# Kernel tuning notes

Measured on AMD Instinct MI355X. Metric: run time of the kernel, lower is better.

Reference implementation:

```python
import jax, jax.numpy as jnp
import numpy as np

N_NODES = 100000

def gcn_conv(h, row, col, w, W, b, n):
    # linear transform then symmetric-normalized weighted aggregation (PyG GCNConv)
    h = h @ W                                   # [N, F_out]
    deg = jax.ops.segment_sum(w, row, num_segments=n)          # weighted in-degree [N]
    dinv = jnp.where(deg > 0, jax.lax.rsqrt(deg), 0.0)
    norm = dinv[row] * w * dinv[col]            # [E]
    msg = norm[:, None] * h[col]                # gather+scale, [E, F_out]
    return jax.ops.segment_sum(msg, row, num_segments=n) + b

def setup_inputs() -> dict:
    key = jax.random.key(0)
    ks = jax.random.split(key, 6)
    N, E, D, H = N_NODES, 1600000, 128, 128
    x = jax.random.normal(ks[0], (N, D), dtype=jnp.float32)
    edge_index = jax.random.randint(ks[1], (2, E), 0, N, dtype=jnp.int64)
    edge_weight = jax.random.uniform(ks[2], (E,), dtype=jnp.float32)
    W1 = jax.random.normal(ks[3], (D, H), dtype=jnp.float32) / np.sqrt(D)
    b1 = jnp.zeros((H,), dtype=jnp.float32)
    W2 = jax.random.normal(ks[4], (H, H), dtype=jnp.float32) / np.sqrt(H)
    b2 = jnp.zeros((H,), dtype=jnp.float32)
    return {"x": x, "edge_index": edge_index, "edge_weight": edge_weight,
            "W1": W1, "b1": b1, "W2": W2, "b2": b2}

def reference(x, edge_index, edge_weight, W1, b1, W2, b2):
    n = x.shape[0]
    # add self-loops with weight 1 (PyG gcn_norm default)
    loops = jnp.arange(n, dtype=edge_index.dtype)
    row = jnp.concatenate([edge_index[0], loops])
    col = jnp.concatenate([edge_index[1], loops])
    w = jnp.concatenate([edge_weight, jnp.ones((n,), dtype=edge_weight.dtype)])
    h = gcn_conv(x, row, col, w, W1, b1, n)
    h = jax.nn.relu(h)  # dropout is identity in eval mode
    h = gcn_conv(h, row, col, w, W2, b2, n)
    return h
```

## Files before the change

kernel.cpp:

```cpp
#include <hip/hip_runtime.h>


constexpr int N_NODES = 100000;
constexpr int FD = 128;
constexpr int NPAD = 100352;
constexpr int CAP = 48;
constexpr int PSH = 7;
constexpr int PROWS = 128;
constexpr int NP = (N_NODES + PROWS - 1) / PROWS;
constexpr int RCAP = 2560;
constexpr int PSTRIDE = 16;
constexpr int EPB = 4096;
constexpr int EPT = 16;

typedef __attribute__((ext_vector_type(8))) short bf16x8;
typedef __attribute__((ext_vector_type(4))) float f32x4;
#define MFMA16(a, b, c) __builtin_amdgcn_mfma_f32_16x16x32_bf16(a, b, c, 0, 0, 0)

static __device__ __forceinline__ unsigned f2bf(float x) {
  unsigned u = __float_as_uint(x);
  return (u + 0x7FFFu + ((u >> 16) & 1u)) >> 16;
}
static __device__ __forceinline__ float bflo(unsigned u) {
  return __uint_as_float(u << 16);
}
static __device__ __forceinline__ float bfhi(unsigned u) {
  return __uint_as_float(u & 0xFFFF0000u);
}

__global__ __launch_bounds__(256) void k_part(const int* __restrict__ row,
                                              const int* __restrict__ col,
                                              const float* __restrict__ w,
                                              int* __restrict__ pcnt,
                                              int2* __restrict__ rec, int E) {
  __shared__ int lcnt[NP];
  const int t = threadIdx.x;
  const int e0 = blockIdx.x * EPB;
  for (int p = t; p < NP; p += 256) lcnt[p] = 0;
  __syncthreads();

  int packed[EPT];
  int cols[EPT];
  int ws[EPT];
#pragma unroll
  for (int i = 0; i < EPT; i++) {
    int e = e0 + i * 256 + t;
    packed[i] = -1;
    if (e < E) {
      int r = row[e];
      cols[i] = col[e];
      ws[i] = __float_as_int(w[e]);
      int part = r >> PSH, rl = r & (PROWS - 1);
      int off = atomicAdd(&lcnt[part], 1);
      packed[i] = part | (rl << 10) | (off << 17);
    }
  }
  __syncthreads();

  for (int p = t; p < NP; p += 256) {
    int c = lcnt[p];
    int base = 0;
    if (c) base = atomicAdd(&pcnt[p * PSTRIDE], c);
    lcnt[p] = base;
  }
  __syncthreads();

#pragma unroll
  for (int i = 0; i < EPT; i++) {
    int pk = packed[i];
    if (pk >= 0) {
      int part = pk & 0x3FF;
      int rl = (pk >> 10) & 0x7F;
      int pos = lcnt[part] + (pk >> 17);
      if (pos < RCAP)
        rec[(size_t)part * RCAP + pos] = make_int2(cols[i] | (rl << 20), ws[i]);
    }
  }
}

__global__ __launch_bounds__(256) void k_bin(const int* __restrict__ pcnt,
                                             const int2* __restrict__ rec,
                                             int2* __restrict__ bucket,
                                             int* __restrict__ cnt,
                                             float* __restrict__ dinv) {
  __shared__ int lcnt[PROWS];
  __shared__ float lsum[PROWS];
  const int part = blockIdx.x, t = threadIdx.x;
  if (t < PROWS) { lcnt[t] = 0; lsum[t] = 0.f; }
  __syncthreads();
  const int n = min(pcnt[part * PSTRIDE], RCAP);
  const int row0 = part << PSH;
  const int2* rp = rec + (size_t)part * RCAP;
  for (int j = t; j < n; j += 256) {
    int2 R = rp[j];
    int rl = R.x >> 20;
    int c = R.x & 0xFFFFF;
    int p = atomicAdd(&lcnt[rl], 1);
    if (p < CAP) bucket[(size_t)(row0 + rl) * CAP + p] = make_int2(c, R.y);
    atomicAdd(&lsum[rl], __int_as_float(R.y));
  }
  __syncthreads();
  int i = row0 + t;
  if (t < PROWS && i < N_NODES) {
    cnt[i] = min(lcnt[t], CAP);
    dinv[i] = rsqrtf(lsum[t] + 1.0f);
  }
}

__global__ __launch_bounds__(128) void k_prep(const float* __restrict__ W1,
                                              const float* __restrict__ W2,
                                              ushort* __restrict__ W1hT,
                                              ushort* __restrict__ W1lT,
                                              ushort* __restrict__ W2hT,
                                              ushort* __restrict__ W2lT) {
  int b = blockIdx.x;
  int n0 = b & (FD - 1);
  int k = threadIdx.x;
  const float* W = (b < FD) ? W1 : W2;
  ushort* Wh = (b < FD) ? W1hT : W2hT;
  ushort* Wl = (b < FD) ? W1lT : W2lT;
  float v = W[k * FD + n0];
  unsigned h = f2bf(v);
  float r = v - bflo(h);
  Wh[n0 * FD + k] = (ushort)h;
  Wl[n0 * FD + k] = (ushort)f2bf(r);
}

__global__ __launch_bounds__(512) void k_gemm(const float* __restrict__ X,
                                              const ushort* __restrict__ WhT,
                                              const ushort* __restrict__ WlT,
                                              const float* __restrict__ dinv,
                                              ushort* __restrict__ Yb,
                                              int relu_in) {
  __shared__ ushort sl[32768];
  ushort* lwh = sl;
  ushort* lwl = sl + 16384;
  const int t = threadIdx.x;
  const int wid = t >> 6;
  const int lane = t & 63;
  const int g = lane >> 4;
  const int lr = lane & 15;

  const size_t row_base = (size_t)blockIdx.x * 128 + wid * 16 + lr;
  const size_t rowc = row_base < N_NODES ? row_base : 0;
  const float* xr = X + rowc * FD;
  float xv[4][8];
#pragma unroll
  for (int ks = 0; ks < 4; ks++) {
    *(float4*)&xv[ks][0] = *(const float4*)(xr + ks * 32 + g * 8);
    *(float4*)&xv[ks][4] = *(const float4*)(xr + ks * 32 + g * 8 + 4);
  }

  {
    const uint4* gh = (const uint4*)WhT;
    const uint4* gl = (const uint4*)WlT;
#pragma unroll
    for (int i = 0; i < 4; i++) {
      int idx = i * 512 + t;
      int byte = idx * 16;
      int n = byte >> 8;
      int swz = byte ^ ((n & 7) << 4);
      *(uint4*)((char*)lwh + swz) = gh[idx];
      *(uint4*)((char*)lwl + swz) = gl[idx];
    }
  }
  __syncthreads();

  f32x4 acc[8];
#pragma unroll
  for (int nf = 0; nf < 8; nf++) acc[nf] = (f32x4)(0.f);

#pragma unroll
  for (int ks = 0; ks < 4; ks++) {
    bf16x8 a_h, a_l;
#pragma unroll
    for (int j = 0; j < 8; j++) {
      float v = xv[ks][j];
      if (relu_in) v = fmaxf(v, 0.f);
      unsigned hb_ = f2bf(v);
      float r = v - bflo(hb_);
      a_h[j] = (short)hb_;
      a_l[j] = (short)f2bf(r);
    }
#pragma unroll
    for (int nf = 0; nf < 8; nf++) {
      int n = nf * 16 + lr;
      int byte = n * 256 + ks * 64 + g * 16;
      int swz = byte ^ ((n & 7) << 4);
      bf16x8 bh = *(const bf16x8*)((const char*)lwh + swz);
      bf16x8 bl = *(const bf16x8*)((const char*)lwl + swz);
      acc[nf] = MFMA16(a_h, bh, acc[nf]);
      acc[nf] = MFMA16(a_l, bh, acc[nf]);
      acc[nf] = MFMA16(a_h, bl, acc[nf]);
    }
  }

  float4 dv = *(const float4*)&dinv[blockIdx.x * 128 + wid * 16 + g * 4];

  __syncthreads();
#pragma unroll
  for (int nf = 0; nf < 8; nf++) {
#pragma unroll
    for (int r = 0; r < 4; r++) {
      int rl = wid * 16 + g * 4 + r;
      int byte = rl * 256 + (nf * 16 + lr) * 2;
      int swz = byte ^ ((rl & 7) << 4);
      *(ushort*)((char*)sl + swz) = (ushort)f2bf(acc[nf][r] * (&dv.x)[r]);
    }
  }
  __syncthreads();
#pragma unroll
  for (int i = 0; i < 4; i++) {
    int idx = i * 512 + t;
    int byte = idx * 16;
    int rl = byte >> 8;
    int swz = byte ^ ((rl & 7) << 4);
    uint4 v = *(const uint4*)((const char*)sl + swz);
    size_t rg = (size_t)blockIdx.x * 128 + rl;
    if (rg < N_NODES) *(uint4*)(Yb + rg * FD + ((byte & 255) >> 1)) = v;
  }
}

static __device__ __forceinline__ void acc8(float* a, float s, uint4 g) {
  a[0] += s * bflo(g.x);
  a[1] += s * bfhi(g.x);
  a[2] += s * bflo(g.y);
  a[3] += s * bfhi(g.y);
  a[4] += s * bflo(g.z);
  a[5] += s * bfhi(g.z);
  a[6] += s * bflo(g.w);
  a[7] += s * bfhi(g.w);
}

__global__ __launch_bounds__(256, 4) void k_gather(
    const ushort* __restrict__ hb, const int* __restrict__ cnt,
    const int2* __restrict__ bucket, const float* __restrict__ dinv,
    const float* __restrict__ b, float* __restrict__ out) {
  int t = blockIdx.x * 256 + threadIdx.x;
  int i = t >> 4, q = t & 15;
  if (i >= N_NODES) return;
  float di = dinv[i];
  const uint4* H = (const uint4*)hb;
  uint4 hv = H[(size_t)i * 16 + q];
  float a[8];
  a[0] = bflo(hv.x); a[1] = bfhi(hv.x);
  a[2] = bflo(hv.y); a[3] = bfhi(hv.y);
  a[4] = bflo(hv.z); a[5] = bfhi(hv.z);
  a[6] = bflo(hv.w); a[7] = bfhi(hv.w);
  const int c = min(cnt[i], CAP);
  const int2* bk = bucket + (size_t)i * CAP;
  const int nb = (c + 7) >> 3;

  int2 cur[8];
  if (nb > 0) {
#pragma unroll
    for (int j = 0; j < 4; j++)
      *(int4*)&cur[j * 2] = *(const int4*)&bk[j * 2];
  }
  for (int bt = 0; bt < nb; bt++) {
    int2 nxt[8];
    if (bt + 1 < nb) {
#pragma unroll
      for (int j = 0; j < 4; j++)
        *(int4*)&nxt[j * 2] = *(const int4*)&bk[(bt + 1) * 8 + j * 2];
    }
    const int base = bt * 8;
    int idx[8];
    float wv[8];
#pragma unroll
    for (int j = 0; j < 8; j++) {
      bool v = (base + j) < c;
      idx[j] = v ? cur[j].x : i;
      wv[j] = v ? __int_as_float(cur[j].y) : 0.f;
    }
    uint4 g[8];
#pragma unroll
    for (int j = 0; j < 8; j++) g[j] = H[(size_t)idx[j] * 16 + q];
#pragma unroll
    for (int j = 0; j < 8; j++) acc8(a, wv[j], g[j]);
#pragma unroll
    for (int j = 0; j < 8; j++) cur[j] = nxt[j];
  }
  float4 b0 = ((const float4*)b)[q * 2];
  float4 b1 = ((const float4*)b)[q * 2 + 1];
  float* o = out + (size_t)i * FD + q * 8;
  float4 o0, o1;
  o0.x = di * a[0] + b0.x; o0.y = di * a[1] + b0.y;
  o0.z = di * a[2] + b0.z; o0.w = di * a[3] + b0.w;
  o1.x = di * a[4] + b1.x; o1.y = di * a[5] + b1.y;
  o1.z = di * a[6] + b1.z; o1.w = di * a[7] + b1.w;
  ((float4*)o)[0] = o0;
  ((float4*)o)[1] = o1;
}

extern "C" void kernel_launch(void* const* d_in, const int* in_sizes, int n_in,
                              void* d_out, int out_size, void* d_ws, size_t ws_size,
                              hipStream_t stream) {
  const float* x  = (const float*)d_in[0];
  const int*   ei = (const int*)d_in[1];
  const float* ew = (const float*)d_in[2];
  const float* W1 = (const float*)d_in[3];
  const float* b1 = (const float*)d_in[4];
  const float* W2 = (const float*)d_in[5];
  const float* b2 = (const float*)d_in[6];
  float* out = (float*)d_out;

  const int E = in_sizes[2];
  const int* row = ei;
  const int* col = ei + E;

  int*    pcnt   = (int*)d_ws;
  float*  dinv   = (float*)(pcnt + 16384);
  int*    cnt    = (int*)(dinv + NPAD);
  int2*   bucket = (int2*)(cnt + NPAD);
  int2*   rec    = bucket + (size_t)NPAD * CAP;
  ushort* hb     = (ushort*)(rec + (size_t)NP * RCAP);
  ushort* w1ht   = hb + (size_t)NPAD * FD;
  ushort* w1lt   = w1ht + FD * FD;
  ushort* w2ht   = w1lt + FD * FD;
  ushort* w2lt   = w2ht + FD * FD;

  hipMemsetAsync(pcnt, 0, 16384 * sizeof(int), stream);
  k_prep<<<2 * FD, FD, 0, stream>>>(W1, W2, w1ht, w1lt, w2ht, w2lt);
  const int part_grid = (E + EPB - 1) / EPB;
  k_part<<<part_grid, 256, 0, stream>>>(row, col, ew, pcnt, rec, E);
  k_bin<<<NP, 256, 0, stream>>>(pcnt, rec, bucket, cnt, dinv);

  const int gemm_grid = (N_NODES + 127) / 128;
  const int ga_grid   = (N_NODES * 16 + 255) / 256;

  k_gemm<<<gemm_grid, 512, 0, stream>>>(x, w1ht, w1lt, dinv, hb, 0);
  k_gather<<<ga_grid, 256, 0, stream>>>(hb, cnt, bucket, dinv, b1, out);
  k_gemm<<<gemm_grid, 512, 0, stream>>>(out, w2ht, w2lt, dinv, hb, 1);
  k_gather<<<ga_grid, 256, 0, stream>>>(hb, cnt, bucket, dinv, b2, out);
}
```

Before: 335.1 us.

## Process two row tiles per GEMM block and store outputs directly with permuted columns

The GEMM kernel now handles 256 rows per block in two 128-row tiles, so each block's weight staging into LDS is reused twice. The B-fragment column mapping is permuted (n = lr*8 + nf) so that each lane holds 8 consecutive output columns. This lets the epilogue pack them into a uint4 and write straight to global memory, removing the LDS staging pass and its two barriers. The separate memset of the partition counters is folded into the weight-prep kernel, dropping one launch. The trade-off is half as many GEMM blocks, which lowers parallelism across CUs.

```diff
diff --git a/kernel.cpp b/kernel.cpp
--- a/kernel.cpp
+++ b/kernel.cpp
@@ -112,10 +112,13 @@
                                               ushort* __restrict__ W1hT,
                                               ushort* __restrict__ W1lT,
                                               ushort* __restrict__ W2hT,
-                                              ushort* __restrict__ W2lT) {
+                                              ushort* __restrict__ W2lT,
+                                              int* __restrict__ pcnt) {
   int b = blockIdx.x;
+  int k = threadIdx.x;
+  int zid = b * 128 + k;
+  if (zid < 16384) pcnt[zid] = 0;
   int n0 = b & (FD - 1);
-  int k = threadIdx.x;
   const float* W = (b < FD) ? W1 : W2;
   ushort* Wh = (b < FD) ? W1hT : W2hT;
   ushort* Wl = (b < FD) ? W1lT : W2lT;
@@ -141,16 +144,6 @@
   const int g = lane >> 4;
   const int lr = lane & 15;
 
-  const size_t row_base = (size_t)blockIdx.x * 128 + wid * 16 + lr;
-  const size_t rowc = row_base < N_NODES ? row_base : 0;
-  const float* xr = X + rowc * FD;
-  float xv[4][8];
-#pragma unroll
-  for (int ks = 0; ks < 4; ks++) {
-    *(float4*)&xv[ks][0] = *(const float4*)(xr + ks * 32 + g * 8);
-    *(float4*)&xv[ks][4] = *(const float4*)(xr + ks * 32 + g * 8 + 4);
-  }
-
   {
     const uint4* gh = (const uint4*)WhT;
     const uint4* gl = (const uint4*)WlT;
@@ -159,65 +152,69 @@
       int idx = i * 512 + t;
       int byte = idx * 16;
       int n = byte >> 8;
-      int swz = byte ^ ((n & 7) << 4);
+      int swz = byte ^ (((n >> 3) & 7) << 4);
       *(uint4*)((char*)lwh + swz) = gh[idx];
       *(uint4*)((char*)lwl + swz) = gl[idx];
     }
   }
   __syncthreads();
 
-  f32x4 acc[8];
-#pragma unroll
-  for (int nf = 0; nf < 8; nf++) acc[nf] = (f32x4)(0.f);
-
-#pragma unroll
-  for (int ks = 0; ks < 4; ks++) {
-    bf16x8 a_h, a_l;
-#pragma unroll
-    for (int j = 0; j < 8; j++) {
-      float v = xv[ks][j];
-      if (relu_in) v = fmaxf(v, 0.f);
-      unsigned hb_ = f2bf(v);
-      float r = v - bflo(hb_);
-      a_h[j] = (short)hb_;
-      a_l[j] = (short)f2bf(r);
-    }
-#pragma unroll
-    for (int nf = 0; nf < 8; nf++) {
-      int n = nf * 16 + lr;
-      int byte = n * 256 + ks * 64 + g * 16;
-      int swz = byte ^ ((n & 7) << 4);
-      bf16x8 bh = *(const bf16x8*)((const char*)lwh + swz);
-      bf16x8 bl = *(const bf16x8*)((const char*)lwl + swz);
-      acc[nf] = MFMA16(a_h, bh, acc[nf]);
-      acc[nf] = MFMA16(a_l, bh, acc[nf]);
-      acc[nf] = MFMA16(a_h, bl, acc[nf]);
-    }
-  }
-
-  float4 dv = *(const float4*)&dinv[blockIdx.x * 128 + wid * 16 + g * 4];
-
-  __syncthreads();
-#pragma unroll
-  for (int nf = 0; nf < 8; nf++) {
+#pragma unroll
+  for (int tile = 0; tile < 2; tile++) {
+    const size_t rb = (size_t)blockIdx.x * 256 + tile * 128;
+    const size_t row_base = rb + wid * 16 + lr;
+    const size_t rowc = row_base < N_NODES ? row_base : 0;
+    const float* xr = X + rowc * FD;
+    float xv[4][8];
+#pragma unroll
+    for (int ks = 0; ks < 4; ks++) {
+      *(float4*)&xv[ks][0] = *(const float4*)(xr + ks * 32 + g * 8);
+      *(float4*)&xv[ks][4] = *(const float4*)(xr + ks * 32 + g * 8 + 4);
+    }
+
+    f32x4 acc[8];
+#pragma unroll
+    for (int nf = 0; nf < 8; nf++) acc[nf] = (f32x4)(0.f);
+
+#pragma unroll
+    for (int ks = 0; ks < 4; ks++) {
+      bf16x8 a_h, a_l;
+#pragma unroll
+      for (int j = 0; j < 8; j++) {
+        float v = xv[ks][j];
+        if (relu_in) v = fmaxf(v, 0.f);
+        unsigned hb_ = f2bf(v);
+        float r = v - bflo(hb_);
+        a_h[j] = (short)hb_;
+        a_l[j] = (short)f2bf(r);
+      }
+#pragma unroll
+      for (int nf = 0; nf < 8; nf++) {
+        int n = lr * 8 + nf;
+        int byte = n * 256 + ks * 64 + g * 16;
+        int swz = byte ^ (((n >> 3) & 7) << 4);
+        bf16x8 bh = *(const bf16x8*)((const char*)lwh + swz);
+        bf16x8 bl = *(const bf16x8*)((const char*)lwl + swz);
+        acc[nf] = MFMA16(a_h, bh, acc[nf]);
+        acc[nf] = MFMA16(a_l, bh, acc[nf]);
+        acc[nf] = MFMA16(a_h, bl, acc[nf]);
+      }
+    }
+
+    const size_t rw = rb + wid * 16;
 #pragma unroll
     for (int r = 0; r < 4; r++) {
-      int rl = wid * 16 + g * 4 + r;
-      int byte = rl * 256 + (nf * 16 + lr) * 2;
-      int swz = byte ^ ((rl & 7) << 4);
-      *(ushort*)((char*)sl + swz) = (ushort)f2bf(acc[nf][r] * (&dv.x)[r]);
-    }
-  }
-  __syncthreads();
-#pragma unroll
-  for (int i = 0; i < 4; i++) {
-    int idx = i * 512 + t;
-    int byte = idx * 16;
-    int rl = byte >> 8;
-    int swz = byte ^ ((rl & 7) << 4);
-    uint4 v = *(const uint4*)((const char*)sl + swz);
-    size_t rg = (size_t)blockIdx.x * 128 + rl;
-    if (rg < N_NODES) *(uint4*)(Yb + rg * FD + ((byte & 255) >> 1)) = v;
+      size_t rg = rw + g * 4 + r;
+      if (rg < N_NODES) {
+        float dv = dinv[rg];
+        uint4 o;
+        o.x = f2bf(acc[0][r] * dv) | (f2bf(acc[1][r] * dv) << 16);
+        o.y = f2bf(acc[2][r] * dv) | (f2bf(acc[3][r] * dv) << 16);
+        o.z = f2bf(acc[4][r] * dv) | (f2bf(acc[5][r] * dv) << 16);
+        o.w = f2bf(acc[6][r] * dv) | (f2bf(acc[7][r] * dv) << 16);
+        *(uint4*)(Yb + rg * FD + lr * 8) = o;
+      }
+    }
   }
 }
 
@@ -320,13 +317,12 @@
   ushort* w2ht   = w1lt + FD * FD;
   ushort* w2lt   = w2ht + FD * FD;
 
-  hipMemsetAsync(pcnt, 0, 16384 * sizeof(int), stream);
-  k_prep<<<2 * FD, FD, 0, stream>>>(W1, W2, w1ht, w1lt, w2ht, w2lt);
+  k_prep<<<2 * FD, FD, 0, stream>>>(W1, W2, w1ht, w1lt, w2ht, w2lt, pcnt);
   const int part_grid = (E + EPB - 1) / EPB;
   k_part<<<part_grid, 256, 0, stream>>>(row, col, ew, pcnt, rec, E);
   k_bin<<<NP, 256, 0, stream>>>(pcnt, rec, bucket, cnt, dinv);
 
-  const int gemm_grid = (N_NODES + 127) / 128;
+  const int gemm_grid = (N_NODES + 255) / 256;
   const int ga_grid   = (N_NODES * 16 + 255) / 256;
 
   k_gemm<<<gemm_grid, 512, 0, stream>>>(x, w1ht, w1lt, dinv, hb, 0);
```

Result: faster. 322.8 us (-3.7%).
